# Kernel tuning notes

Measured on AMD Instinct MI355X. Metric: run time of the kernel, lower is better.

Reference implementation:

```python
import jax, jax.numpy as jnp
import numpy as np

B, S, D = 4, 4096, 1024
E, H, TOPK = 8, 2752, 2


def setup_inputs() -> dict:
    key = jax.random.key(0)
    k0, k1, k2, k3, k4 = jax.random.split(key, 5)
    x = jax.random.normal(k0, (B, S, D), dtype=jnp.float32)
    gate_w = jax.random.normal(k1, (E, D), dtype=jnp.float32) * 0.02
    w1 = jax.random.normal(k2, (E, H, D), dtype=jnp.float32) * 0.02
    w2 = jax.random.normal(k3, (E, D, H), dtype=jnp.float32) * 0.02
    w3 = jax.random.normal(k4, (E, H, D), dtype=jnp.float32) * 0.02
    return {"x": x, "gate_w": gate_w, "w1": w1, "w2": w2, "w3": w3}


def reference(x, gate_w, w1, w2, w3):
    """MoE layer: softmax router -> top-k (normalized) -> per-expert SwiGLU FFN -> weighted combine."""
    b, s, d = x.shape
    xt = x.reshape(-1, d)                       # [T, D], T = B*S
    logits = xt @ gate_w.T                      # [T, E]
    scores = jax.nn.softmax(logits, axis=-1)
    topk_w, topk_i = jax.lax.top_k(scores, TOPK)  # [T, K]
    topk_w = topk_w / (jnp.sum(topk_w, axis=-1, keepdims=True) + 1e-20)

    y = jnp.zeros_like(xt)
    n_experts = gate_w.shape[0]
    for e in range(n_experts):
        # combine weight for expert e per token (0 if not routed to e)
        we = jnp.sum(jnp.where(topk_i == e, topk_w, 0.0), axis=-1)  # [T]
        h = jax.nn.silu(xt @ w1[e].T) * (xt @ w3[e].T)              # [T, H]
        y = y + we[:, None] * (h @ w2[e].T)                         # [T, D]
    return y.reshape(b, s, d)
```

## Files before the change

### kernel.cpp

```cpp
#include <hip/hip_runtime.h>
#include <hip/hip_bf16.h>
#include <stdint.h>

#define T_TOK 16384
#define D_DIM 1024
#define E_NUM 8
#define H_DIM 2752
#define NSLOT (T_TOK * 2)

typedef __bf16 bf16x8_t __attribute__((ext_vector_type(8)));
typedef float f32x4_t __attribute__((ext_vector_type(4)));

__device__ __forceinline__ uint16_t f2bf(float f) {
    union { float f; uint32_t u; } v; v.f = f;
    return (uint16_t)((v.u + 0x7FFFu + ((v.u >> 16) & 1u)) >> 16);
}
__device__ __forceinline__ ushort4 f4_to_bf4(float4 v) {
    ushort4 r; r.x = f2bf(v.x); r.y = f2bf(v.y); r.z = f2bf(v.z); r.w = f2bf(v.w);
    return r;
}
__device__ __forceinline__ void gl_lds16(const uint16_t* g, uint16_t* l) {
    __builtin_amdgcn_global_load_lds((const __attribute__((address_space(1))) void*)g,
                                     (__attribute__((address_space(3))) void*)l,
                                     16, 0, 0);
}

__global__ __launch_bounds__(256) void router_kernel(
    const float* __restrict__ x, const float* __restrict__ gw,
    int* __restrict__ topk_i, float* __restrict__ topk_w) {
    int tid = threadIdx.x;
    int t = blockIdx.x * 4 + (tid >> 6);
    int lane = tid & 63;
    const float* xr = x + (size_t)t * D_DIM;
    double acc[E_NUM];
#pragma unroll
    for (int e = 0; e < E_NUM; ++e) acc[e] = 0.0;
    for (int k = lane; k < D_DIM; k += 64) {
        double xv = (double)xr[k];
#pragma unroll
        for (int e = 0; e < E_NUM; ++e) acc[e] += xv * (double)gw[e * D_DIM + k];
    }
#pragma unroll
    for (int e = 0; e < E_NUM; ++e) {
        double v = acc[e];
        for (int off = 32; off > 0; off >>= 1) v += __shfl_down(v, off, 64);
        acc[e] = v;
    }
    if (lane == 0) {
        int i0 = 0; double m0 = acc[0];
#pragma unroll
        for (int e = 1; e < E_NUM; ++e) if (acc[e] > m0) { m0 = acc[e]; i0 = e; }
        int i1 = -1; double m1 = -1.0e300;
#pragma unroll
        for (int e = 0; e < E_NUM; ++e) if (e != i0 && acc[e] > m1) { m1 = acc[e]; i1 = e; }
        double e1 = exp(m1 - m0);
        double s = 1.0 + e1;
        topk_i[t * 2 + 0] = i0; topk_i[t * 2 + 1] = i1;
        topk_w[t * 2 + 0] = (float)(1.0 / s);
        topk_w[t * 2 + 1] = (float)(e1 / s);
    }
}

__global__ __launch_bounds__(256) void count_kernel(
    const int* __restrict__ topk_i,
    int* __restrict__ counts_f, int* __restrict__ counts_s) {
    __shared__ int hf[E_NUM], hs[E_NUM];
    int tid = threadIdx.x;
    if (tid < E_NUM) { hf[tid] = 0; hs[tid] = 0; }
    __syncthreads();
    int t = blockIdx.x * 256 + tid;
    atomicAdd(&hf[topk_i[t * 2 + 0]], 1);
    atomicAdd(&hs[topk_i[t * 2 + 1]], 1);
    __syncthreads();
    if (tid < E_NUM) {
        if (hf[tid]) atomicAdd(&counts_f[tid], hf[tid]);
    } else if (tid < 2 * E_NUM) {
        int e = tid - E_NUM;
        if (hs[e]) atomicAdd(&counts_s[e], hs[e]);
    }
}

__global__ void prefix_kernel(const int* __restrict__ cf, const int* __restrict__ cs,
                              int* __restrict__ bases, int* __restrict__ splits,
                              int* __restrict__ cnts) {
    int s = 0;
    for (int e = 0; e < E_NUM; ++e) {
        bases[e] = s;
        splits[e] = s + cf[e];
        cnts[e] = cf[e] + cs[e];
        s += cnts[e];
    }
}

__global__ __launch_bounds__(256) void assign_kernel(
    const int* __restrict__ topk_i, const float* __restrict__ topk_w,
    const int* __restrict__ bases, const int* __restrict__ splits,
    int* __restrict__ fills_f, int* __restrict__ fills_s,
    int* __restrict__ slot_tok, float* __restrict__ slot_w) {
    __shared__ int hf[E_NUM], hs[E_NUM], bf[E_NUM], bs[E_NUM];
    int tid = threadIdx.x;
    if (tid < E_NUM) { hf[tid] = 0; hs[tid] = 0; }
    __syncthreads();
    int t = blockIdx.x * 256 + tid;
    int e0 = topk_i[t * 2 + 0], e1 = topk_i[t * 2 + 1];
    int r0 = atomicAdd(&hf[e0], 1);
    int r1 = atomicAdd(&hs[e1], 1);
    __syncthreads();
    if (tid < E_NUM) {
        bf[tid] = hf[tid] ? atomicAdd(&fills_f[tid], hf[tid]) : 0;
    } else if (tid < 2 * E_NUM) {
        int e = tid - E_NUM;
        bs[e] = hs[e] ? atomicAdd(&fills_s[e], hs[e]) : 0;
    }
    __syncthreads();
    int s0 = bases[e0] + bf[e0] + r0;
    int s1 = splits[e1] + bs[e1] + r1;
    slot_tok[s0] = t; slot_w[s0] = topk_w[t * 2 + 0];
    slot_tok[s1] = t; slot_w[s1] = topk_w[t * 2 + 1];
}

__global__ __launch_bounds__(256) void cvtx_kernel(const float* __restrict__ x,
                                                   uint16_t* __restrict__ Xb) {
    size_t i = (size_t)blockIdx.x * 256 + threadIdx.x;
    ((ushort4*)Xb)[i] = f4_to_bf4(((const float4*)x)[i]);
}
__global__ __launch_bounds__(256) void cvt13_kernel(const float* __restrict__ w1,
                                                    const float* __restrict__ w3,
                                                    uint16_t* __restrict__ w1be,
                                                    uint16_t* __restrict__ w3be, int e) {
    size_t i = (size_t)blockIdx.x * 256 + threadIdx.x;
    const float4* s1 = (const float4*)(w1 + (size_t)e * H_DIM * D_DIM);
    const float4* s3 = (const float4*)(w3 + (size_t)e * H_DIM * D_DIM);
    ((ushort4*)w1be)[i] = f4_to_bf4(s1[i]);
    ((ushort4*)w3be)[i] = f4_to_bf4(s3[i]);
}
__global__ __launch_bounds__(256) void cvt2_kernel(const float* __restrict__ w2,
                                                   uint16_t* __restrict__ w2b) {
    size_t i = (size_t)blockIdx.x * 256 + threadIdx.x;
    ((ushort4*)w2b)[i] = f4_to_bf4(((const float4*)w2)[i]);
}

__global__ __launch_bounds__(256) void gemm1_kernel(
    const uint16_t* __restrict__ Xb, const uint16_t* __restrict__ w1be,
    const uint16_t* __restrict__ w3be, const int* __restrict__ slot_tok,
    const int* __restrict__ cnts, const int* __restrict__ bases,
    uint16_t* __restrict__ hidden, int e) {
    int cnt = cnts[e];
    int m0 = blockIdx.y * 128;
    if (m0 >= cnt) return;
    int n0 = blockIdx.x * 64;
    int base = bases[e];

    __shared__ __align__(16) uint16_t As[128 * 32];
    __shared__ __align__(16) uint16_t B1s[64 * 32];
    __shared__ __align__(16) uint16_t B3s[64 * 32];

    int tid = threadIdx.x;
    int w = tid >> 6, lane = tid & 63;
    int rA = lane & 15, kq = lane >> 4;
    int lr = lane >> 2, lc = lane & 3;

    int tok0 = slot_tok[base + min(m0 + w * 32 + lr, cnt - 1)];
    int tok1 = slot_tok[base + min(m0 + w * 32 + 16 + lr, cnt - 1)];
    const uint16_t* pA0 = Xb + (size_t)tok0 * D_DIM + lc * 8;
    const uint16_t* pA1 = Xb + (size_t)tok1 * D_DIM + lc * 8;
    const uint16_t* pB1 = w1be + (size_t)(n0 + w * 16 + lr) * D_DIM + lc * 8;
    const uint16_t* pB3 = w3be + (size_t)(n0 + w * 16 + lr) * D_DIM + lc * 8;
    uint16_t* lA0 = &As[(w * 2 + 0) * 512];
    uint16_t* lA1 = &As[(w * 2 + 1) * 512];
    uint16_t* lB1 = &B1s[w * 512];
    uint16_t* lB3 = &B3s[w * 512];

    f32x4_t acc1[2][4], acc3[2][4];
#pragma unroll
    for (int r = 0; r < 2; ++r)
#pragma unroll
        for (int n = 0; n < 4; ++n) {
            acc1[r][n] = (f32x4_t){0.f, 0.f, 0.f, 0.f};
            acc3[r][n] = (f32x4_t){0.f, 0.f, 0.f, 0.f};
        }

    for (int k0 = 0; k0 < D_DIM; k0 += 32) {
        __syncthreads();
        gl_lds16(pA0, lA0);
        gl_lds16(pA1, lA1);
        gl_lds16(pB1, lB1);
        gl_lds16(pB3, lB3);
        pA0 += 32; pA1 += 32; pB1 += 32; pB3 += 32;
        __syncthreads();

        bf16x8_t a0 = *(const bf16x8_t*)&As[(w * 32 + rA) * 32 + kq * 8];
        bf16x8_t a1 = *(const bf16x8_t*)&As[(w * 32 + 16 + rA) * 32 + kq * 8];
#pragma unroll
        for (int n = 0; n < 4; ++n) {
            bf16x8_t b1 = *(const bf16x8_t*)&B1s[(n * 16 + rA) * 32 + kq * 8];
            bf16x8_t b3 = *(const bf16x8_t*)&B3s[(n * 16 + rA) * 32 + kq * 8];
            acc1[0][n] = __builtin_amdgcn_mfma_f32_16x16x32_bf16(a0, b1, acc1[0][n], 0, 0, 0);
            acc1[1][n] = __builtin_amdgcn_mfma_f32_16x16x32_bf16(a1, b1, acc1[1][n], 0, 0, 0);
            acc3[0][n] = __builtin_amdgcn_mfma_f32_16x16x32_bf16(a0, b3, acc3[0][n], 0, 0, 0);
            acc3[1][n] = __builtin_amdgcn_mfma_f32_16x16x32_bf16(a1, b3, acc3[1][n], 0, 0, 0);
        }
    }

#pragma unroll
    for (int r = 0; r < 2; ++r)
#pragma unroll
        for (int n = 0; n < 4; ++n)
#pragma unroll
            for (int i = 0; i < 4; ++i) {
                int mrow = m0 + w * 32 + r * 16 + kq * 4 + i;
                if (mrow < cnt) {
                    float g = acc1[r][n][i];
                    float s = g / (1.0f + __expf(-g));
                    float h = s * acc3[r][n][i];
                    hidden[(size_t)(base + mrow) * H_DIM + n0 + n * 16 + rA] = f2bf(h);
                }
            }
}

__global__ __launch_bounds__(256) void gemm2_kernel(
    const uint16_t* __restrict__ hidden, const uint16_t* __restrict__ w2b,
    const int* __restrict__ cnts, const int* __restrict__ bases,
    const int* __restrict__ splits, const int* __restrict__ slot_tok,
    const float* __restrict__ slot_w, float* __restrict__ out, int pass) {
    int e = blockIdx.z;
    int cnt = cnts[e];
    int m0 = blockIdx.y * 128;
    if (m0 >= cnt) return;
    int base = bases[e];
    int split = splits[e];
    if (pass == 0 && base + m0 >= split) return;
    if (pass == 1 && base + m0 + 128 <= split) return;
    int d0 = blockIdx.x * 128;

    __shared__ __align__(16) uint16_t As[128 * 32];
    __shared__ __align__(16) uint16_t Bs[128 * 32];

    int tid = threadIdx.x;
    int w = tid >> 6, lane = tid & 63;
    int rA = lane & 15, kq = lane >> 4;
    int lr = lane >> 2, lc = lane & 3;
    int mh = w & 1, nh = w >> 1;

    int sl0 = base + min(m0 + w * 32 + lr, cnt - 1);
    int sl1 = base + min(m0 + w * 32 + 16 + lr, cnt - 1);
    const uint16_t* pA0 = hidden + (size_t)sl0 * H_DIM + lc * 8;
    const uint16_t* pA1 = hidden + (size_t)sl1 * H_DIM + lc * 8;
    const uint16_t* pB0 = w2b + (size_t)(e * D_DIM + d0 + w * 32 + lr) * H_DIM + lc * 8;
    const uint16_t* pB1 = w2b + (size_t)(e * D_DIM + d0 + w * 32 + 16 + lr) * H_DIM + lc * 8;
    uint16_t* lA0 = &As[(w * 2 + 0) * 512];
    uint16_t* lA1 = &As[(w * 2 + 1) * 512];
    uint16_t* lB0 = &Bs[(w * 2 + 0) * 512];
    uint16_t* lB1 = &Bs[(w * 2 + 1) * 512];

    f32x4_t acc[4][4];
#pragma unroll
    for (int mf = 0; mf < 4; ++mf)
#pragma unroll
        for (int nf = 0; nf < 4; ++nf) acc[mf][nf] = (f32x4_t){0.f, 0.f, 0.f, 0.f};

    for (int k0 = 0; k0 < H_DIM; k0 += 32) {
        __syncthreads();
        gl_lds16(pA0, lA0);
        gl_lds16(pA1, lA1);
        gl_lds16(pB0, lB0);
        gl_lds16(pB1, lB1);
        pA0 += 32; pA1 += 32; pB0 += 32; pB1 += 32;
        __syncthreads();

        bf16x8_t a[4], b[4];
#pragma unroll
        for (int mf = 0; mf < 4; ++mf)
            a[mf] = *(const bf16x8_t*)&As[(mh * 64 + mf * 16 + rA) * 32 + kq * 8];
#pragma unroll
        for (int nf = 0; nf < 4; ++nf)
            b[nf] = *(const bf16x8_t*)&Bs[(nh * 64 + nf * 16 + rA) * 32 + kq * 8];
#pragma unroll
        for (int mf = 0; mf < 4; ++mf)
#pragma unroll
            for (int nf = 0; nf < 4; ++nf)
                acc[mf][nf] = __builtin_amdgcn_mfma_f32_16x16x32_bf16(a[mf], b[nf], acc[mf][nf], 0, 0, 0);
    }

#pragma unroll
    for (int mf = 0; mf < 4; ++mf)
#pragma unroll
        for (int i = 0; i < 4; ++i) {
            int mr = m0 + mh * 64 + mf * 16 + kq * 4 + i;
            if (mr < cnt) {
                int slot = base + mr;
                bool isfirst = slot < split;
                if ((pass == 0) == isfirst) {
                    float wgt = slot_w[slot];
                    int tok = slot_tok[slot];
                    float* yr = out + (size_t)tok * D_DIM + d0 + nh * 64;
                    if (pass == 0) {
#pragma unroll
                        for (int nf = 0; nf < 4; ++nf)
                            yr[nf * 16 + rA] = wgt * acc[mf][nf][i];
                    } else {
#pragma unroll
                        for (int nf = 0; nf < 4; ++nf)
                            yr[nf * 16 + rA] += wgt * acc[mf][nf][i];
                    }
                }
            }
        }
}

extern "C" void kernel_launch(void* const* d_in, const int* in_sizes, int n_in,
                              void* d_out, int out_size, void* d_ws, size_t ws_size,
                              hipStream_t stream) {
    const float* x  = (const float*)d_in[0];
    const float* gw = (const float*)d_in[1];
    const float* w1 = (const float*)d_in[2];
    const float* w2 = (const float*)d_in[3];
    const float* w3 = (const float*)d_in[4];
    float* out = (float*)d_out;
    char* ws = (char*)d_ws;

    int*   counts_f = (int*)(ws + 0);
    int*   counts_s = (int*)(ws + 256);
    int*   fills_f  = (int*)(ws + 512);
    int*   fills_s  = (int*)(ws + 768);
    int*   bases    = (int*)(ws + 1024);
    int*   splits   = (int*)(ws + 1280);
    int*   cnts     = (int*)(ws + 1536);
    int*   topk_i   = (int*)(ws + 4096);
    float* topk_w   = (float*)(ws + 4096 + 1 * 131072);
    int*   slot_tok = (int*)(ws + 4096 + 2 * 131072);
    float* slot_w   = (float*)(ws + 4096 + 3 * 131072);

    const size_t HID_OFF = 4ull << 20;
    const size_t W_OFF   = HID_OFF + (size_t)NSLOT * H_DIM * 2;
    const size_t W1SZ    = (size_t)H_DIM * D_DIM * 2;
    uint16_t* hidden = (uint16_t*)(ws + HID_OFF);
    uint16_t* w1be   = (uint16_t*)(ws + W_OFF);
    uint16_t* w3be   = (uint16_t*)(ws + W_OFF + W1SZ);
    uint16_t* Xb     = (uint16_t*)(ws + W_OFF + 2 * W1SZ);
    uint16_t* w2b    = (uint16_t*)(ws + W_OFF);

    hipMemsetAsync(ws, 0, 1024, stream);

    router_kernel<<<T_TOK / 4, 256, 0, stream>>>(x, gw, topk_i, topk_w);
    count_kernel<<<T_TOK / 256, 256, 0, stream>>>(topk_i, counts_f, counts_s);
    prefix_kernel<<<1, 1, 0, stream>>>(counts_f, counts_s, bases, splits, cnts);
    assign_kernel<<<T_TOK / 256, 256, 0, stream>>>(topk_i, topk_w, bases, splits,
                                                   fills_f, fills_s, slot_tok, slot_w);
    cvtx_kernel<<<T_TOK * D_DIM / 1024, 256, 0, stream>>>(x, Xb);

    for (int e = 0; e < E_NUM; ++e) {
        cvt13_kernel<<<H_DIM, 256, 0, stream>>>(w1, w3, w1be, w3be, e);
        gemm1_kernel<<<dim3(H_DIM / 64, 128), 256, 0, stream>>>(
            Xb, w1be, w3be, slot_tok, cnts, bases, hidden, e);
    }

    cvt2_kernel<<<E_NUM * D_DIM * H_DIM / 1024, 256, 0, stream>>>(w2, w2b);
    gemm2_kernel<<<dim3(D_DIM / 128, 128, E_NUM), 256, 0, stream>>>(
        hidden, w2b, cnts, bases, splits, slot_tok, slot_w, out, 0);
    gemm2_kernel<<<dim3(D_DIM / 128, 128, E_NUM), 256, 0, stream>>>(
        hidden, w2b, cnts, bases, splits, slot_tok, slot_w, out, 1);
}
```

Measured before the change: 1.307 ms.

## Double-buffer LDS tiles and swizzle block order in both expert GEMMs

Both expert GEMM kernels now keep two shared-memory buffers. Each iteration issues the global-to-LDS loads for the next K-slice before computing on the current one, which removes one barrier per iteration and lets memory traffic overlap the MFMA work. The linear block index is also remapped so that neighbouring workgroups share the same weight or activation tiles, aiming at better L2 reuse. The cost is twice the LDS per block, which may lower occupancy, and the swizzle hardcodes the grid shape.

```diff
diff --git a/kernel.cpp b/kernel.cpp
--- a/kernel.cpp
+++ b/kernel.cpp
@@ -146,14 +146,17 @@
     const int* __restrict__ cnts, const int* __restrict__ bases,
     uint16_t* __restrict__ hidden, int e) {
     int cnt = cnts[e];
-    int m0 = blockIdx.y * 128;
+    int lin = blockIdx.y * 43 + blockIdx.x;
+    int swz = (lin & 7) * 688 + (lin >> 3);
+    int m_t = swz / 43, n_t = swz % 43;
+    int m0 = m_t * 128;
     if (m0 >= cnt) return;
-    int n0 = blockIdx.x * 64;
+    int n0 = n_t * 64;
     int base = bases[e];
 
-    __shared__ __align__(16) uint16_t As[128 * 32];
-    __shared__ __align__(16) uint16_t B1s[64 * 32];
-    __shared__ __align__(16) uint16_t B3s[64 * 32];
+    __shared__ __align__(16) uint16_t As[2][128 * 32];
+    __shared__ __align__(16) uint16_t B1s[2][64 * 32];
+    __shared__ __align__(16) uint16_t B3s[2][64 * 32];
 
     int tid = threadIdx.x;
     int w = tid >> 6, lane = tid & 63;
@@ -166,10 +169,6 @@
     const uint16_t* pA1 = Xb + (size_t)tok1 * D_DIM + lc * 8;
     const uint16_t* pB1 = w1be + (size_t)(n0 + w * 16 + lr) * D_DIM + lc * 8;
     const uint16_t* pB3 = w3be + (size_t)(n0 + w * 16 + lr) * D_DIM + lc * 8;
-    uint16_t* lA0 = &As[(w * 2 + 0) * 512];
-    uint16_t* lA1 = &As[(w * 2 + 1) * 512];
-    uint16_t* lB1 = &B1s[w * 512];
-    uint16_t* lB3 = &B3s[w * 512];
 
     f32x4_t acc1[2][4], acc3[2][4];
 #pragma unroll
@@ -180,26 +179,37 @@
             acc3[r][n] = (f32x4_t){0.f, 0.f, 0.f, 0.f};
         }
 
+    {
+        gl_lds16(pA0, &As[0][(w * 2 + 0) * 512]);
+        gl_lds16(pA1, &As[0][(w * 2 + 1) * 512]);
+        gl_lds16(pB1, &B1s[0][w * 512]);
+        gl_lds16(pB3, &B3s[0][w * 512]);
+        pA0 += 32; pA1 += 32; pB1 += 32; pB3 += 32;
+    }
+    int cur = 0;
     for (int k0 = 0; k0 < D_DIM; k0 += 32) {
         __syncthreads();
-        gl_lds16(pA0, lA0);
-        gl_lds16(pA1, lA1);
-        gl_lds16(pB1, lB1);
-        gl_lds16(pB3, lB3);
-        pA0 += 32; pA1 += 32; pB1 += 32; pB3 += 32;
-        __syncthreads();
-
-        bf16x8_t a0 = *(const bf16x8_t*)&As[(w * 32 + rA) * 32 + kq * 8];
-        bf16x8_t a1 = *(const bf16x8_t*)&As[(w * 32 + 16 + rA) * 32 + kq * 8];
+        if (k0 + 32 < D_DIM) {
+            int nb = cur ^ 1;
+            gl_lds16(pA0, &As[nb][(w * 2 + 0) * 512]);
+            gl_lds16(pA1, &As[nb][(w * 2 + 1) * 512]);
+            gl_lds16(pB1, &B1s[nb][w * 512]);
+            gl_lds16(pB3, &B3s[nb][w * 512]);
+            pA0 += 32; pA1 += 32; pB1 += 32; pB3 += 32;
+        }
+
+        bf16x8_t a0 = *(const bf16x8_t*)&As[cur][(w * 32 + rA) * 32 + kq * 8];
+        bf16x8_t a1 = *(const bf16x8_t*)&As[cur][(w * 32 + 16 + rA) * 32 + kq * 8];
 #pragma unroll
         for (int n = 0; n < 4; ++n) {
-            bf16x8_t b1 = *(const bf16x8_t*)&B1s[(n * 16 + rA) * 32 + kq * 8];
-            bf16x8_t b3 = *(const bf16x8_t*)&B3s[(n * 16 + rA) * 32 + kq * 8];
+            bf16x8_t b1 = *(const bf16x8_t*)&B1s[cur][(n * 16 + rA) * 32 + kq * 8];
+            bf16x8_t b3 = *(const bf16x8_t*)&B3s[cur][(n * 16 + rA) * 32 + kq * 8];
             acc1[0][n] = __builtin_amdgcn_mfma_f32_16x16x32_bf16(a0, b1, acc1[0][n], 0, 0, 0);
             acc1[1][n] = __builtin_amdgcn_mfma_f32_16x16x32_bf16(a1, b1, acc1[1][n], 0, 0, 0);
             acc3[0][n] = __builtin_amdgcn_mfma_f32_16x16x32_bf16(a0, b3, acc3[0][n], 0, 0, 0);
             acc3[1][n] = __builtin_amdgcn_mfma_f32_16x16x32_bf16(a1, b3, acc3[1][n], 0, 0, 0);
         }
+        cur ^= 1;
     }
 
 #pragma unroll
@@ -225,16 +235,19 @@
     const float* __restrict__ slot_w, float* __restrict__ out, int pass) {
     int e = blockIdx.z;
     int cnt = cnts[e];
-    int m0 = blockIdx.y * 128;
+    int lin = blockIdx.y * 8 + blockIdx.x;
+    int swz = (lin & 7) * 128 + (lin >> 3);
+    int y_t = swz >> 3, x_t = swz & 7;
+    int m0 = y_t * 128;
     if (m0 >= cnt) return;
     int base = bases[e];
     int split = splits[e];
     if (pass == 0 && base + m0 >= split) return;
     if (pass == 1 && base + m0 + 128 <= split) return;
-    int d0 = blockIdx.x * 128;
-
-    __shared__ __align__(16) uint16_t As[128 * 32];
-    __shared__ __align__(16) uint16_t Bs[128 * 32];
+    int d0 = x_t * 128;
+
+    __shared__ __align__(16) uint16_t As[2][128 * 32];
+    __shared__ __align__(16) uint16_t Bs[2][128 * 32];
 
     int tid = threadIdx.x;
     int w = tid >> 6, lane = tid & 63;
@@ -248,10 +261,6 @@
     const uint16_t* pA1 = hidden + (size_t)sl1 * H_DIM + lc * 8;
     const uint16_t* pB0 = w2b + (size_t)(e * D_DIM + d0 + w * 32 + lr) * H_DIM + lc * 8;
     const uint16_t* pB1 = w2b + (size_t)(e * D_DIM + d0 + w * 32 + 16 + lr) * H_DIM + lc * 8;
-    uint16_t* lA0 = &As[(w * 2 + 0) * 512];
-    uint16_t* lA1 = &As[(w * 2 + 1) * 512];
-    uint16_t* lB0 = &Bs[(w * 2 + 0) * 512];
-    uint16_t* lB1 = &Bs[(w * 2 + 1) * 512];
 
     f32x4_t acc[4][4];
 #pragma unroll
@@ -259,27 +268,38 @@
 #pragma unroll
         for (int nf = 0; nf < 4; ++nf) acc[mf][nf] = (f32x4_t){0.f, 0.f, 0.f, 0.f};
 
+    {
+        gl_lds16(pA0, &As[0][(w * 2 + 0) * 512]);
+        gl_lds16(pA1, &As[0][(w * 2 + 1) * 512]);
+        gl_lds16(pB0, &Bs[0][(w * 2 + 0) * 512]);
+        gl_lds16(pB1, &Bs[0][(w * 2 + 1) * 512]);
+        pA0 += 32; pA1 += 32; pB0 += 32; pB1 += 32;
+    }
+    int cur = 0;
     for (int k0 = 0; k0 < H_DIM; k0 += 32) {
         __syncthreads();
-        gl_lds16(pA0, lA0);
-        gl_lds16(pA1, lA1);
-        gl_lds16(pB0, lB0);
-        gl_lds16(pB1, lB1);
-        pA0 += 32; pA1 += 32; pB0 += 32; pB1 += 32;
-        __syncthreads();
+        if (k0 + 32 < H_DIM) {
+            int nb = cur ^ 1;
+            gl_lds16(pA0, &As[nb][(w * 2 + 0) * 512]);
+            gl_lds16(pA1, &As[nb][(w * 2 + 1) * 512]);
+            gl_lds16(pB0, &Bs[nb][(w * 2 + 0) * 512]);
+            gl_lds16(pB1, &Bs[nb][(w * 2 + 1) * 512]);
+            pA0 += 32; pA1 += 32; pB0 += 32; pB1 += 32;
+        }
 
         bf16x8_t a[4], b[4];
 #pragma unroll
         for (int mf = 0; mf < 4; ++mf)
-            a[mf] = *(const bf16x8_t*)&As[(mh * 64 + mf * 16 + rA) * 32 + kq * 8];
+            a[mf] = *(const bf16x8_t*)&As[cur][(mh * 64 + mf * 16 + rA) * 32 + kq * 8];
 #pragma unroll
         for (int nf = 0; nf < 4; ++nf)
-            b[nf] = *(const bf16x8_t*)&Bs[(nh * 64 + nf * 16 + rA) * 32 + kq * 8];
+            b[nf] = *(const bf16x8_t*)&Bs[cur][(nh * 64 + nf * 16 + rA) * 32 + kq * 8];
 #pragma unroll
         for (int mf = 0; mf < 4; ++mf)
 #pragma unroll
             for (int nf = 0; nf < 4; ++nf)
                 acc[mf][nf] = __builtin_amdgcn_mfma_f32_16x16x32_bf16(a[mf], b[nf], acc[mf][nf], 0, 0, 0);
+        cur ^= 1;
     }
 
 #pragma unroll
```

Measured after the change: 4.362 ms. +233.8%, slower.

## Merge two-pass gemm2 into one atomic-accumulate launch and remap tile order

Applied to the files above, without the earlier changes.

The second GEMM no longer runs as two passes (store for first-choice slots, then read-add for second-choice slots). It becomes a single launch that zeroes the output with a memset and accumulates weighted results with float atomicAdd. Both GEMM kernels also remap block indices so that groups of 8 consecutive blocks share the same weight column tile across different token tiles, aiming for better cache reuse of weights. The atomics add global contention and make the floating-point summation order nondeterministic, and the memset adds a full output write.

```diff
diff --git a/kernel.cpp b/kernel.cpp
--- a/kernel.cpp
+++ b/kernel.cpp
@@ -146,9 +146,13 @@
     const int* __restrict__ cnts, const int* __restrict__ bases,
     uint16_t* __restrict__ hidden, int e) {
     int cnt = cnts[e];
-    int m0 = blockIdx.y * 128;
+    int lin = blockIdx.y * 43 + blockIdx.x;
+    int c = lin & 7, j = lin >> 3;
+    int m_t = (j / 43) * 8 + c;
+    int n_t = j % 43;
+    int m0 = m_t * 128;
     if (m0 >= cnt) return;
-    int n0 = blockIdx.x * 64;
+    int n0 = n_t * 64;
     int base = bases[e];
 
     __shared__ __align__(16) uint16_t As[128 * 32];
@@ -221,17 +225,18 @@
 __global__ __launch_bounds__(256) void gemm2_kernel(
     const uint16_t* __restrict__ hidden, const uint16_t* __restrict__ w2b,
     const int* __restrict__ cnts, const int* __restrict__ bases,
-    const int* __restrict__ splits, const int* __restrict__ slot_tok,
-    const float* __restrict__ slot_w, float* __restrict__ out, int pass) {
+    const int* __restrict__ slot_tok, const float* __restrict__ slot_w,
+    float* __restrict__ out) {
     int e = blockIdx.z;
     int cnt = cnts[e];
-    int m0 = blockIdx.y * 128;
+    int lin = blockIdx.y * 8 + blockIdx.x;
+    int c = lin & 7, j = lin >> 3;
+    int m_t = (j >> 3) * 8 + c;
+    int x_t = j & 7;
+    int m0 = m_t * 128;
     if (m0 >= cnt) return;
     int base = bases[e];
-    int split = splits[e];
-    if (pass == 0 && base + m0 >= split) return;
-    if (pass == 1 && base + m0 + 128 <= split) return;
-    int d0 = blockIdx.x * 128;
+    int d0 = x_t * 128;
 
     __shared__ __align__(16) uint16_t As[128 * 32];
     __shared__ __align__(16) uint16_t Bs[128 * 32];
@@ -289,21 +294,12 @@
             int mr = m0 + mh * 64 + mf * 16 + kq * 4 + i;
             if (mr < cnt) {
                 int slot = base + mr;
-                bool isfirst = slot < split;
-                if ((pass == 0) == isfirst) {
-                    float wgt = slot_w[slot];
-                    int tok = slot_tok[slot];
-                    float* yr = out + (size_t)tok * D_DIM + d0 + nh * 64;
-                    if (pass == 0) {
-#pragma unroll
-                        for (int nf = 0; nf < 4; ++nf)
-                            yr[nf * 16 + rA] = wgt * acc[mf][nf][i];
-                    } else {
-#pragma unroll
-                        for (int nf = 0; nf < 4; ++nf)
-                            yr[nf * 16 + rA] += wgt * acc[mf][nf][i];
-                    }
-                }
+                float wgt = slot_w[slot];
+                int tok = slot_tok[slot];
+                float* yr = out + (size_t)tok * D_DIM + d0 + nh * 64;
+#pragma unroll
+                for (int nf = 0; nf < 4; ++nf)
+                    atomicAdd(&yr[nf * 16 + rA], wgt * acc[mf][nf][i]);
             }
         }
 }
@@ -341,6 +337,7 @@
     uint16_t* w2b    = (uint16_t*)(ws + W_OFF);
 
     hipMemsetAsync(ws, 0, 1024, stream);
+    hipMemsetAsync(out, 0, (size_t)T_TOK * D_DIM * sizeof(float), stream);
 
     router_kernel<<<T_TOK / 4, 256, 0, stream>>>(x, gw, topk_i, topk_w);
     count_kernel<<<T_TOK / 256, 256, 0, stream>>>(topk_i, counts_f, counts_s);
@@ -356,8 +353,6 @@
     }
 
     cvt2_kernel<<<E_NUM * D_DIM * H_DIM / 1024, 256, 0, stream>>>(w2, w2b);
-    gemm2_kernel<<<dim3(D_DIM / 128, 128, E_NUM), 256, 0, stream>>>(
-        hidden, w2b, cnts, bases, splits, slot_tok, slot_w, out, 0);
-    gemm2_kernel<<<dim3(D_DIM / 128, 128, E_NUM), 256, 0, stream>>>(
-        hidden, w2b, cnts, bases, splits, slot_tok, slot_w, out, 1);
-}
+    gemm2_kernel<<<dim3(8, 128, E_NUM), 256, 0, stream>>>(
+        hidden, w2b, cnts, bases, slot_tok, slot_w, out);
+}
```

New measurement: 1.358 ms. 3.9% more time.
